# Optimization experiments

Measured on AMD Instinct MI355X. Metric: run time of the kernel, lower is better.

## Reference

```python
import jax, jax.numpy as jnp
import numpy as np
from jax import lax

H_IMG = 128; W_IMG = 128; C_IN = 200; NCLS = 16
N0 = H_IMG * W_IMG; N1 = 4096; N2 = 1024
K = 16  # neighbors(15) + 1 self loop, as in __init__
EPS = 1e-5
SLOPE = 0.01  # LeakyReLU default


def _leaky(x):
    return jnp.where(x >= 0, x, SLOPE * x)


def _bn1d(H, g, b):
    # BatchNorm1d in training mode: batch stats over node dim
    mu = H.mean(0)
    var = H.var(0)
    return (H - mu) * lax.rsqrt(var + EPS) * g + b


def _bn2d(x, g, b):
    mu = x.mean((0, 2, 3), keepdims=True)
    var = x.var((0, 2, 3), keepdims=True)
    return (x - mu) * lax.rsqrt(var + EPS) * g[None, :, None, None] + b[None, :, None, None]


def _ssconv(x, g, b, pw, pb, dw, db):
    # BN -> 1x1 pointwise conv -> LeakyReLU -> depthwise 5x5 conv -> LeakyReLU
    y = _bn2d(x, g, b)
    y = lax.conv_general_dilated(y, pw, (1, 1), 'SAME', dimension_numbers=('NCHW', 'OIHW', 'NCHW')) + pb[None, :, None, None]
    y = _leaky(y)
    c = dw.shape[0]
    y = lax.conv_general_dilated(y, dw, (1, 1), 'SAME', feature_group_count=c, dimension_numbers=('NCHW', 'OIHW', 'NCHW')) + db[None, :, None, None]
    return _leaky(y)


def _gcn(H, g, b, wt, bt, wo, bo, nbr):
    # GCNLayer_PyG, neighbors>0 branch. nbr: [N, K] neighbor indices (col), center broadcast (row)
    Hn = _bn1d(H, g, b)
    th = Hn @ wt + bt            # [N, 128]
    out = Hn @ wo + bo           # [N, F]
    A = jax.nn.sigmoid(jnp.einsum('nkd,nd->nk', th[nbr], th))  # sigmoid(<theta[col], theta[row]>)
    A = jax.nn.softmax(A, axis=1)                              # softmax over K neighbors
    agg = jnp.einsum('nk,nkf->nf', A, out[nbr])                # weighted neighbor aggregate
    return _leaky(agg), A


def _forward(x, hg, hb, hpw, hpb, hdw, hdb,
             e0_g, e0_b, e0_wt, e0_bt, e0_wo, e0_bo,
             e1_g, e1_b, e1_wt, e1_bt, e1_wo, e1_bo,
             d0_g, d0_b, d0_wt, d0_bt, d0_wo, d0_bo,
             tg, tb, tpw, tpb, tdw, tdb, ws, wb,
             S0, S1, Shat0, Shat1, nbr_a, nbr_b):
    x4 = x.transpose(2, 0, 1)[None]                 # [1, C, H, W]
    h0 = _ssconv(x4, hg, hb, hpw, hpb, hdw, hdb)    # [1, 128, H, W]
    H = h0[0].transpose(1, 2, 0).reshape(N0, -1)    # [N0, 128]
    enc0 = H
    H = Shat0 @ H                                   # pool to [N1, 128]
    H, A0 = _gcn(H, e0_g, e0_b, e0_wt, e0_bt, e0_wo, e0_bo, nbr_a)  # [N1, 64]
    enc1 = H
    H = Shat1 @ H                                   # pool to [N2, 64]
    H, A1 = _gcn(H, e1_g, e1_b, e1_wt, e1_bt, e1_wo, e1_bo, nbr_b)  # [N2, 32]
    # decoder
    H = S1 @ H                                      # unpool [N1, 32]
    H = jnp.concatenate([H, enc1], axis=-1)         # [N1, 96]
    H, Ad = _gcn(H, d0_g, d0_b, d0_wt, d0_bt, d0_wo, d0_bo, nbr_a)  # [N1, 64]
    H = S0 @ H                                      # unpool [N0, 64]
    H = jnp.concatenate([H, enc0], axis=-1)         # [N0, 192]
    t = H.reshape(1, H_IMG, W_IMG, -1).transpose(0, 3, 1, 2)
    f = _ssconv(t, tg, tb, tpw, tpb, tdw, tdb)      # [1, 128, H, W]
    f = f[0].transpose(1, 2, 0).reshape(N0, -1)
    Y = jax.nn.softmax(f @ ws + wb, axis=-1)        # [N0, NCLS]
    return Y


def setup_inputs() -> dict:
    key = jax.random.key(0)
    cnt = [0]
    def rn(shape, s=0.05):
        cnt[0] += 1
        return jax.random.normal(jax.random.fold_in(key, cnt[0]), shape, jnp.float32) * s
    x = rn((H_IMG, W_IMG, C_IN), 1.0)
    # balanced hierarchical assignment matrices (one-hot rows)
    S0 = jnp.zeros((N0, N1), jnp.float32).at[jnp.arange(N0), jnp.arange(N0) // (N0 // N1)].set(1.0)
    S1 = jnp.zeros((N1, N2), jnp.float32).at[jnp.arange(N1), jnp.arange(N1) // (N1 // N2)].set(1.0)
    Shat0 = (S0 / S0.sum(0, keepdims=True)).T
    Shat1 = (S1 / S1.sum(0, keepdims=True)).T
    # positions: pixel grid pooled through Shat (as in HiGCN.__init__)
    gx, gy = jnp.meshgrid(jnp.arange(H_IMG), jnp.arange(W_IMG), indexing='ij')
    pos = jnp.stack([gx, gy], -1).reshape(N0, 2).astype(jnp.float32)
    posA = Shat0 @ pos
    posB = Shat1 @ posA
    def knn(p):
        d = ((p[:, None, :] - p[None, :, :]) ** 2).sum(-1)
        return jnp.argsort(d, axis=1)[:, :K].astype(jnp.int32)  # self included (loop=True)
    nbr_a = knn(posA)  # [N1, K], used by enc0 and dec0
    nbr_b = knn(posB)  # [N2, K], used by enc1
    inp = dict(x=x, S0=S0, S1=S1, Shat0=Shat0, Shat1=Shat1, nbr_a=nbr_a, nbr_b=nbr_b)
    inp.update(hg=jnp.ones(C_IN), hb=jnp.zeros(C_IN), hpw=rn((128, C_IN, 1, 1)),
               hpb=jnp.zeros(128), hdw=rn((128, 1, 5, 5)), hdb=jnp.zeros(128))
    for tag, ci, co in (('e0', 128, 64), ('e1', 64, 32), ('d0', 96, 64)):
        inp[tag + '_g'] = jnp.ones(ci); inp[tag + '_b'] = jnp.zeros(ci)
        inp[tag + '_wt'] = rn((ci, 128)); inp[tag + '_bt'] = jnp.zeros(128)
        inp[tag + '_wo'] = rn((ci, co)); inp[tag + '_bo'] = jnp.zeros(co)
    inp.update(tg=jnp.ones(192), tb=jnp.zeros(192), tpw=rn((128, 192, 1, 1)),
               tpb=jnp.zeros(128), tdw=rn((128, 1, 5, 5)), tdb=jnp.zeros(128))
    inp.update(ws=rn((128, NCLS)), wb=jnp.zeros(NCLS))
    return inp


def reference(x, hg, hb, hpw, hpb, hdw, hdb,
              e0_g, e0_b, e0_wt, e0_bt, e0_wo, e0_bo,
              e1_g, e1_b, e1_wt, e1_bt, e1_wo, e1_bo,
              d0_g, d0_b, d0_wt, d0_bt, d0_wo, d0_bo,
              tg, tb, tpw, tpb, tdw, tdb, ws, wb,
              S0, S1, Shat0, Shat1, nbr_a, nbr_b):
    return _forward(x, hg, hb, hpw, hpb, hdw, hdb,
                    e0_g, e0_b, e0_wt, e0_bt, e0_wo, e0_bo,
                    e1_g, e1_b, e1_wt, e1_bt, e1_wo, e1_bo,
                    d0_g, d0_b, d0_wt, d0_bt, d0_wo, d0_bo,
                    tg, tb, tpw, tpb, tdw, tdb, ws, wb,
                    S0, S1, Shat0, Shat1, nbr_a, nbr_b)
```

## Files before the change

kernel.cpp:

```cpp
#include <hip/hip_runtime.h>
#include <hip/hip_bf16.h>
#include <math.h>

using bf16 = __hip_bfloat16;

#define H_IMG 128
#define W_IMG 128
#define C_IN  200
#define NCLS  16
#define N0    16384
#define N1    4096
#define N2    1024
#define KNB   16
#define EPS   1e-5f
#define SLOPE 0.01f

__device__ __forceinline__ float ldf(const float* p, long i) { return p[i]; }
__device__ __forceinline__ float ldf(const bf16* p, long i) { return __bfloat162float(p[i]); }
__device__ __forceinline__ float leaky(float v) { return v >= 0.f ? v : SLOPE * v; }

__device__ __forceinline__ float4 ld4(const float* p, long i) {
    return *reinterpret_cast<const float4*>(p + i);
}
__device__ __forceinline__ float4 ld4(const bf16* p, long i) {
    const ushort4 u = *reinterpret_cast<const ushort4*>(reinterpret_cast<const unsigned short*>(p) + i);
    float4 r;
    r.x = __uint_as_float((unsigned)u.x << 16);
    r.y = __uint_as_float((unsigned)u.y << 16);
    r.z = __uint_as_float((unsigned)u.z << 16);
    r.w = __uint_as_float((unsigned)u.w << 16);
    return r;
}

__global__ void detect_kernel(const unsigned short* __restrict__ x, int* __restrict__ flag) {
    int t = threadIdx.x;
    int cnt = 0;
    for (int i = t; i < 4096; i += 64) {
        unsigned short e = (unsigned short)((x[i] >> 7) & 0xFF);
        if (e >= 0xC0) cnt++;
    }
#pragma unroll
    for (int off = 32; off > 0; off >>= 1) cnt += __shfl_xor(cnt, off, 64);
    if (t == 0) *flag = (cnt > 32) ? 1 : 0;
}

template <typename TX>
__device__ __forceinline__ void bnA_body(const TX* __restrict__ X, int P, int C, float* __restrict__ part) {
    int b = blockIdx.x;
    int t = threadIdx.x;
    int rpb = P >> 8;
    if (t < C) {
        float s = 0.f, s2 = 0.f;
        long base = (long)b * rpb * C + t;
        for (int r = 0; r < rpb; r++) {
            float v = ldf(X, base + (long)r * C);
            s += v; s2 += v * v;
        }
        part[(long)t * 256 + b] = s;
        part[65536 + (long)t * 256 + b] = s2;
    }
}

__global__ __launch_bounds__(256) void bnA_kernel(const void* X, int P, int C, float* part,
                                                  const int* flag, int xraw) {
    if (*flag || !xraw) bnA_body<float>((const float*)X, P, C, part);
    else bnA_body<bf16>((const bf16*)X, P, C, part);
}

__global__ __launch_bounds__(256) void bnB_kernel(const float* __restrict__ part, int P,
                                                  const void* g, const void* b_,
                                                  float* __restrict__ alpha, float* __restrict__ beta,
                                                  const int* flag) {
    int c = blockIdx.x;
    int t = threadIdx.x;
    __shared__ float rs[256], rq[256];
    rs[t] = part[(long)c * 256 + t];
    rq[t] = part[65536 + (long)c * 256 + t];
    __syncthreads();
    for (int k = 128; k > 0; k >>= 1) {
        if (t < k) { rs[t] += rs[t + k]; rq[t] += rq[t + k]; }
        __syncthreads();
    }
    if (t == 0) {
        float mu = rs[0] / (float)P;
        float var = rq[0] / (float)P - mu * mu;
        float gv = *flag ? ((const float*)g)[c] : __bfloat162float(((const bf16*)g)[c]);
        float bv = *flag ? ((const float*)b_)[c] : __bfloat162float(((const bf16*)b_)[c]);
        float a = rsqrtf(var + EPS) * gv;
        alpha[c] = a;
        beta[c] = bv - mu * a;
    }
}

template <typename TW>
__device__ __forceinline__ void fold_body(const TW* __restrict__ W, const TW* __restrict__ bias,
                                          const float* __restrict__ alpha, const float* __restrict__ beta,
                                          float* __restrict__ Wf, float* __restrict__ Bf,
                                          int Ci, int Co, int omajor, int j) {
    int t = threadIdx.x;
    float acc = 0.f;
    for (int c = t; c < Ci; c += 256) {
        float w = omajor ? ldf(W, (long)j * Ci + c) : ldf(W, (long)c * Co + j);
        Wf[(long)c * Co + j] = w * alpha[c];
        acc += w * beta[c];
    }
    __shared__ float red[256];
    red[t] = acc; __syncthreads();
    for (int k = 128; k > 0; k >>= 1) { if (t < k) red[t] += red[t + k]; __syncthreads(); }
    if (t == 0) Bf[j] = ldf(bias, (long)j) + red[0];
}

__global__ __launch_bounds__(256) void fold_kernel(const void* W, const void* bias,
                                                   const float* alpha, const float* beta,
                                                   float* Wf, float* Bf, int Ci, int Co, int omajor,
                                                   const int* flag) {
    if (*flag) fold_body<float>((const float*)W, (const float*)bias, alpha, beta, Wf, Bf, Ci, Co, omajor, blockIdx.x);
    else fold_body<bf16>((const bf16*)W, (const bf16*)bias, alpha, beta, Wf, Bf, Ci, Co, omajor, blockIdx.x);
}

__global__ __launch_bounds__(256) void fold2_kernel(const void* W1, const void* b1,
                                                    const void* W2, const void* b2,
                                                    const float* alpha, const float* beta,
                                                    float* Wf1, float* Bf1, float* Wf2, float* Bf2,
                                                    int Ci, int Co1, int Co2, const int* flag) {
    int j = blockIdx.x;
    if (*flag) {
        if (j < Co1) fold_body<float>((const float*)W1, (const float*)b1, alpha, beta, Wf1, Bf1, Ci, Co1, 0, j);
        else fold_body<float>((const float*)W2, (const float*)b2, alpha, beta, Wf2, Bf2, Ci, Co2, 0, j - Co1);
    } else {
        if (j < Co1) fold_body<bf16>((const bf16*)W1, (const bf16*)b1, alpha, beta, Wf1, Bf1, Ci, Co1, 0, j);
        else fold_body<bf16>((const bf16*)W2, (const bf16*)b2, alpha, beta, Wf2, Bf2, Ci, Co2, 0, j - Co1);
    }
}

template <typename T, int ACT>
__device__ __forceinline__ void gemm4_body(const T* __restrict__ In, const float* __restrict__ Wf,
                                           const float* __restrict__ Bf, float* __restrict__ Out,
                                           int Ci, int Co, int blk) {
    int tid = blk * 256 + threadIdx.x;
    int Coq = Co >> 2;
    int n = tid / Coq;
    int j4 = (tid - n * Coq) << 2;
    const T* in = In + (long)n * Ci;
    const float* wp = Wf + j4;
    float4 acc = *reinterpret_cast<const float4*>(Bf + j4);
    for (int c = 0; c < Ci; c += 4) {
        float4 xv = ld4(in, c);
        float4 w0 = *reinterpret_cast<const float4*>(wp + (long)c * Co);
        float4 w1 = *reinterpret_cast<const float4*>(wp + (long)(c + 1) * Co);
        float4 w2 = *reinterpret_cast<const float4*>(wp + (long)(c + 2) * Co);
        float4 w3 = *reinterpret_cast<const float4*>(wp + (long)(c + 3) * Co);
        acc.x += xv.x * w0.x; acc.y += xv.x * w0.y; acc.z += xv.x * w0.z; acc.w += xv.x * w0.w;
        acc.x += xv.y * w1.x; acc.y += xv.y * w1.y; acc.z += xv.y * w1.z; acc.w += xv.y * w1.w;
        acc.x += xv.z * w2.x; acc.y += xv.z * w2.y; acc.z += xv.z * w2.z; acc.w += xv.z * w2.w;
        acc.x += xv.w * w3.x; acc.y += xv.w * w3.y; acc.z += xv.w * w3.z; acc.w += xv.w * w3.w;
    }
    if (ACT) { acc.x = leaky(acc.x); acc.y = leaky(acc.y); acc.z = leaky(acc.z); acc.w = leaky(acc.w); }
    *reinterpret_cast<float4*>(Out + (long)n * Co + j4) = acc;
}

__global__ __launch_bounds__(256) void gemm4_dyn_kernel(const void* In, const float* Wf, const float* Bf,
                                                        float* Out, int Ci, int Co, const int* flag) {
    if (*flag) gemm4_body<float, 1>((const float*)In, Wf, Bf, Out, Ci, Co, blockIdx.x);
    else gemm4_body<bf16, 1>((const bf16*)In, Wf, Bf, Out, Ci, Co, blockIdx.x);
}

template <int ACT>
__global__ __launch_bounds__(256) void gemm4_f32_kernel(const float* In, const float* Wf, const float* Bf,
                                                        float* Out, int Ci, int Co) {
    gemm4_body<float, ACT>(In, Wf, Bf, Out, Ci, Co, blockIdx.x);
}

template <int ACT>
__global__ __launch_bounds__(256) void gemm2_f32_kernel(const float* In,
                                                        const float* W1, const float* B1, float* O1, int Co1,
                                                        const float* W2, const float* B2, float* O2, int Co2,
                                                        int Ci, int nb1) {
    int b = blockIdx.x;
    if (b < nb1) gemm4_body<float, ACT>(In, W1, B1, O1, Ci, Co1, b);
    else gemm4_body<float, ACT>(In, W2, B2, O2, Ci, Co2, b - nb1);
}

template <typename TW>
__device__ __forceinline__ void dw4_body(const float* __restrict__ In, const TW* __restrict__ dwp,
                                         const TW* __restrict__ dbp, float* __restrict__ Out) {
    __shared__ float wl[25][128];
    __shared__ float bl[128];
    int t = threadIdx.x;
    for (int e = t; e < 25 * 128; e += 256) {
        int o = e / 25, i = e - o * 25;
        wl[i][o] = ldf(dwp, e);
    }
    if (t < 128) bl[t] = ldf(dbp, (long)t);
    __syncthreads();

    int tid = blockIdx.x * 256 + t;
    int o0 = (tid & 31) << 2;
    int p = tid >> 5;
    int h = p >> 7, w = p & 127;
    float4 acc = *reinterpret_cast<const float4*>(&bl[o0]);
#pragma unroll
    for (int dh = -2; dh <= 2; dh++) {
        int hh = h + dh;
        if ((unsigned)hh >= (unsigned)H_IMG) continue;
#pragma unroll
        for (int dv = -2; dv <= 2; dv++) {
            int ww = w + dv;
            if ((unsigned)ww >= (unsigned)W_IMG) continue;
            float4 iv = *reinterpret_cast<const float4*>(&In[(long)(((hh << 7) + ww) << 7) + o0]);
            float4 wv = *reinterpret_cast<const float4*>(&wl[(dh + 2) * 5 + (dv + 2)][o0]);
            acc.x += iv.x * wv.x; acc.y += iv.y * wv.y; acc.z += iv.z * wv.z; acc.w += iv.w * wv.w;
        }
    }
    acc.x = leaky(acc.x); acc.y = leaky(acc.y); acc.z = leaky(acc.z); acc.w = leaky(acc.w);
    *reinterpret_cast<float4*>(&Out[(long)p * 128 + o0]) = acc;
}

__global__ __launch_bounds__(256) void dw4_kernel(const float* In, const void* dwp, const void* dbp,
                                                  float* Out, const int* flag) {
    if (*flag) dw4_body<float>(In, (const float*)dwp, (const float*)dbp, Out);
    else dw4_body<bf16>(In, (const bf16*)dwp, (const bf16*)dbp, Out);
}

__global__ __launch_bounds__(256) void pool4_kernel(const float* __restrict__ In, float* __restrict__ Out, int F) {
    int tid = blockIdx.x * 256 + threadIdx.x;
    int Fq = F >> 2;
    int j = tid / Fq;
    int f4 = (tid - j * Fq) << 2;
    const float* base = In + (long)(4 * j) * F + f4;
    float4 a = *reinterpret_cast<const float4*>(base);
    float4 b = *reinterpret_cast<const float4*>(base + F);
    float4 c = *reinterpret_cast<const float4*>(base + 2 * F);
    float4 d = *reinterpret_cast<const float4*>(base + 3 * F);
    float4 r;
    r.x = 0.25f * (a.x + b.x + c.x + d.x);
    r.y = 0.25f * (a.y + b.y + c.y + d.y);
    r.z = 0.25f * (a.z + b.z + c.z + d.z);
    r.w = 0.25f * (a.w + b.w + c.w + d.w);
    *reinterpret_cast<float4*>(Out + (long)j * F + f4) = r;
}

__global__ __launch_bounds__(256) void attn_kernel(const float* __restrict__ th, const float* __restrict__ outm,
                                                   const int* __restrict__ nbr, float* __restrict__ dst, int co) {
    int n = blockIdx.x * 4 + (threadIdx.x >> 6);
    int l = threadIdx.x & 63;
    float r0 = th[(long)n * 128 + l];
    float r1 = th[(long)n * 128 + 64 + l];
    int mk[KNB];
    float av[KNB];
#pragma unroll
    for (int k = 0; k < KNB; k++) {
        int m = nbr[n * KNB + k];
        mk[k] = m;
        float v = r0 * th[(long)m * 128 + l] + r1 * th[(long)m * 128 + 64 + l];
#pragma unroll
        for (int off = 32; off > 0; off >>= 1) v += __shfl_xor(v, off, 64);
        av[k] = 1.f / (1.f + expf(-v));
    }
    float amax = av[0];
#pragma unroll
    for (int k = 1; k < KNB; k++) amax = fmaxf(amax, av[k]);
    float den = 0.f;
#pragma unroll
    for (int k = 0; k < KNB; k++) { av[k] = expf(av[k] - amax); den += av[k]; }
    float rden = 1.f / den;
    if (l < co) {
        float acc = 0.f;
#pragma unroll
        for (int k = 0; k < KNB; k++) acc += av[k] * outm[(long)mk[k] * co + l];
        dst[(long)n * co + l] = leaky(acc * rden);
    }
}

__global__ __launch_bounds__(256) void concat_hcat_kernel(const float* __restrict__ Hd, const float* __restrict__ enc1,
                                                          float* __restrict__ Hcat) {
    int tid = blockIdx.x * 256 + threadIdx.x;
    int n = tid / 24;
    int f4 = (tid - n * 24) << 2;
    float4 v;
    if (f4 < 32) v = *reinterpret_cast<const float4*>(&Hd[(long)(n >> 2) * 32 + f4]);
    else v = *reinterpret_cast<const float4*>(&enc1[(long)n * 64 + (f4 - 32)]);
    *reinterpret_cast<float4*>(&Hcat[(long)n * 96 + f4]) = v;
}

__global__ __launch_bounds__(256) void concat_g_kernel(const float* __restrict__ Hdec, const float* __restrict__ H0,
                                                       float* __restrict__ G) {
    int tid = blockIdx.x * 256 + threadIdx.x;
    int p = tid / 48;
    int f4 = (tid - p * 48) << 2;
    float4 v;
    if (f4 < 64) v = *reinterpret_cast<const float4*>(&Hdec[(long)(p >> 2) * 64 + f4]);
    else v = *reinterpret_cast<const float4*>(&H0[(long)p * 128 + (f4 - 64)]);
    *reinterpret_cast<float4*>(&G[(long)p * 192 + f4]) = v;
}

template <typename TW>
__device__ __forceinline__ void cls_body(const float* __restrict__ F, const TW* __restrict__ wsw,
                                         const TW* __restrict__ wb, TW* __restrict__ out) {
    __shared__ float wl[128 * 16];
    int t = threadIdx.x;
    for (int e = t; e < 2048; e += 256) wl[e] = ldf(wsw, (long)e);
    __syncthreads();
    int tid = blockIdx.x * 256 + t;
    int p = tid >> 4;
    int j = tid & 15;
    float acc = ldf(wb, (long)j);
    const float* fp = F + (long)p * 128;
#pragma unroll 8
    for (int c = 0; c < 128; c += 4) {
        float4 fv = *reinterpret_cast<const float4*>(fp + c);
        acc += fv.x * wl[c * 16 + j] + fv.y * wl[(c + 1) * 16 + j]
             + fv.z * wl[(c + 2) * 16 + j] + fv.w * wl[(c + 3) * 16 + j];
    }
    float m = acc;
#pragma unroll
    for (int s = 8; s > 0; s >>= 1) m = fmaxf(m, __shfl_xor(m, s, 16));
    float e = expf(acc - m);
    float d = e;
#pragma unroll
    for (int s = 8; s > 0; s >>= 1) d += __shfl_xor(d, s, 16);
    float r = e / d;
    if constexpr (sizeof(TW) == 2) out[tid] = __float2bfloat16(r);
    else out[tid] = r;
}

__global__ __launch_bounds__(256) void cls_kernel(const float* F, const void* wsw, const void* wb,
                                                  void* out, const int* flag) {
    if (*flag) cls_body<float>(F, (const float*)wsw, (const float*)wb, (float*)out);
    else cls_body<bf16>(F, (const bf16*)wsw, (const bf16*)wb, (bf16*)out);
}

extern "C" void kernel_launch(void* const* d_in, const int* in_sizes, int n_in,
                              void* d_out, int out_size, void* d_ws, size_t ws_size,
                              hipStream_t stream) {
    bool dict = (in_sizes[1] > 1000000);
    int I_x, I_nbr_a, I_nbr_b, I_hg, I_ws, I_e0, I_e1, I_d0, I_tg;
    if (dict) {
        I_x = 0; I_nbr_a = 5; I_nbr_b = 6; I_hg = 7; I_e0 = 13; I_e1 = 19; I_d0 = 25; I_tg = 31; I_ws = 37;
    } else {
        I_x = 0; I_hg = 1; I_e0 = 7; I_e1 = 13; I_d0 = 19; I_tg = 25; I_ws = 31; I_nbr_a = 37; I_nbr_b = 38;
    }
    const void* x    = d_in[I_x];
    const int* nbr_a = (const int*)d_in[I_nbr_a];
    const int* nbr_b = (const int*)d_in[I_nbr_b];
    const void* hg   = d_in[I_hg + 0];
    const void* hb   = d_in[I_hg + 1];
    const void* hpw  = d_in[I_hg + 2];
    const void* hpb  = d_in[I_hg + 3];
    const void* hdw  = d_in[I_hg + 4];
    const void* hdb  = d_in[I_hg + 5];
    const void* e0_g = d_in[I_e0 + 0];
    const void* e0_b = d_in[I_e0 + 1];
    const void* e0_wt= d_in[I_e0 + 2];
    const void* e0_bt= d_in[I_e0 + 3];
    const void* e0_wo= d_in[I_e0 + 4];
    const void* e0_bo= d_in[I_e0 + 5];
    const void* e1_g = d_in[I_e1 + 0];
    const void* e1_b = d_in[I_e1 + 1];
    const void* e1_wt= d_in[I_e1 + 2];
    const void* e1_bt= d_in[I_e1 + 3];
    const void* e1_wo= d_in[I_e1 + 4];
    const void* e1_bo= d_in[I_e1 + 5];
    const void* d0_g = d_in[I_d0 + 0];
    const void* d0_b = d_in[I_d0 + 1];
    const void* d0_wt= d_in[I_d0 + 2];
    const void* d0_bt= d_in[I_d0 + 3];
    const void* d0_wo= d_in[I_d0 + 4];
    const void* d0_bo= d_in[I_d0 + 5];
    const void* tg   = d_in[I_tg + 0];
    const void* tb   = d_in[I_tg + 1];
    const void* tpw  = d_in[I_tg + 2];
    const void* tpb  = d_in[I_tg + 3];
    const void* tdw  = d_in[I_tg + 4];
    const void* tdb  = d_in[I_tg + 5];
    const void* wsw  = d_in[I_ws + 0];
    const void* wb   = d_in[I_ws + 1];

    float* W = (float*)d_ws;
    float* AB_a  = W + 0;
    float* AB_b  = W + 256;
    float* WF1   = W + 512;
    float* BF1   = W + 33280;
    float* WF2   = W + 33536;
    float* BF2   = W + 41728;
    int*   dflag = (int*)(W + 49152);
    float* PART  = W + 49408;
    float* R0    = W + 196608;
    float* R1    = R0 + (long)N0*192;
    float* H1b   = R1 + (long)N0*128;
    float* THb   = H1b + (long)N1*128;
    float* OUTb  = THb + (long)N1*128;
    float* ENC1  = OUTb + (long)N1*64;
    float* H2b   = ENC1 + (long)N1*64;
    float* HDb   = H2b + (long)N2*64;
    float* HCAT  = HDb + (long)N2*32;
    float* HDEC  = HCAT + (long)N1*96;

    detect_kernel<<<1, 64, 0, stream>>>((const unsigned short*)x, dflag);

    bnA_kernel<<<256, 256, 0, stream>>>(x, N0, C_IN, PART, dflag, 1);
    bnB_kernel<<<C_IN, 256, 0, stream>>>(PART, N0, hg, hb, AB_a, AB_b, dflag);
    fold_kernel<<<128, 256, 0, stream>>>(hpw, hpb, AB_a, AB_b, WF1, BF1, C_IN, 128, 1, dflag);
    gemm4_dyn_kernel<<<(N0 * 128 / 4) / 256, 256, 0, stream>>>(x, WF1, BF1, R0, C_IN, 128, dflag);
    dw4_kernel<<<(N0 * 32) / 256, 256, 0, stream>>>(R0, hdw, hdb, R1, dflag);
    pool4_kernel<<<(N1 * 32) / 256, 256, 0, stream>>>(R1, H1b, 128);

    bnA_kernel<<<256, 256, 0, stream>>>(H1b, N1, 128, PART, dflag, 0);
    bnB_kernel<<<128, 256, 0, stream>>>(PART, N1, e0_g, e0_b, AB_a, AB_b, dflag);
    fold2_kernel<<<192, 256, 0, stream>>>(e0_wt, e0_bt, e0_wo, e0_bo, AB_a, AB_b,
                                          WF1, BF1, WF2, BF2, 128, 128, 64, dflag);
    {
        int nb1 = (N1 * 32) / 256, nb2 = (N1 * 16) / 256;
        gemm2_f32_kernel<0><<<nb1 + nb2, 256, 0, stream>>>(H1b, WF1, BF1, THb, 128,
                                                           WF2, BF2, OUTb, 64, 128, nb1);
    }
    attn_kernel<<<N1 / 4, 256, 0, stream>>>(THb, OUTb, nbr_a, ENC1, 64);
    pool4_kernel<<<(N2 * 16) / 256, 256, 0, stream>>>(ENC1, H2b, 64);

    bnA_kernel<<<256, 256, 0, stream>>>(H2b, N2, 64, PART, dflag, 0);
    bnB_kernel<<<64, 256, 0, stream>>>(PART, N2, e1_g, e1_b, AB_a, AB_b, dflag);
    fold2_kernel<<<160, 256, 0, stream>>>(e1_wt, e1_bt, e1_wo, e1_bo, AB_a, AB_b,
                                          WF1, BF1, WF2, BF2, 64, 128, 32, dflag);
    {
        int nb1 = (N2 * 32) / 256, nb2 = (N2 * 8) / 256;
        gemm2_f32_kernel<0><<<nb1 + nb2, 256, 0, stream>>>(H2b, WF1, BF1, THb, 128,
                                                           WF2, BF2, OUTb, 32, 64, nb1);
    }
    attn_kernel<<<N2 / 4, 256, 0, stream>>>(THb, OUTb, nbr_b, HDb, 32);

    concat_hcat_kernel<<<(N1 * 24) / 256, 256, 0, stream>>>(HDb, ENC1, HCAT);
    bnA_kernel<<<256, 256, 0, stream>>>(HCAT, N1, 96, PART, dflag, 0);
    bnB_kernel<<<96, 256, 0, stream>>>(PART, N1, d0_g, d0_b, AB_a, AB_b, dflag);
    fold2_kernel<<<192, 256, 0, stream>>>(d0_wt, d0_bt, d0_wo, d0_bo, AB_a, AB_b,
                                          WF1, BF1, WF2, BF2, 96, 128, 64, dflag);
    {
        int nb1 = (N1 * 32) / 256, nb2 = (N1 * 16) / 256;
        gemm2_f32_kernel<0><<<nb1 + nb2, 256, 0, stream>>>(HCAT, WF1, BF1, THb, 128,
                                                           WF2, BF2, OUTb, 64, 96, nb1);
    }
    attn_kernel<<<N1 / 4, 256, 0, stream>>>(THb, OUTb, nbr_a, HDEC, 64);

    concat_g_kernel<<<(N0 * 48) / 256, 256, 0, stream>>>(HDEC, R1, R0);
    bnA_kernel<<<256, 256, 0, stream>>>(R0, N0, 192, PART, dflag, 0);
    bnB_kernel<<<192, 256, 0, stream>>>(PART, N0, tg, tb, AB_a, AB_b, dflag);
    fold_kernel<<<128, 256, 0, stream>>>(tpw, tpb, AB_a, AB_b, WF1, BF1, 192, 128, 1, dflag);
    gemm4_f32_kernel<1><<<(N0 * 128 / 4) / 256, 256, 0, stream>>>(R0, WF1, BF1, R1, 192, 128);
    dw4_kernel<<<(N0 * 32) / 256, 256, 0, stream>>>(R1, tdw, tdb, R0, dflag);
    cls_kernel<<<(N0 * NCLS) / 256, 256, 0, stream>>>(R0, wsw, wb, d_out, dflag);
}
```

Before: 841.2 us.

## Fuse BN statistics into producers, fold concats into GEMMs, cut launches

Computes BatchNorm partial sums inside the kernels that produce each tensor: pooling, attention, and the input read, which now also does dtype detection. It merges the stats reduction with the weight-fold kernels. The two concat kernels are removed by letting the GEMMs read from two source buffers, with the upsampled part indexed by n>>2. The aim is fewer launches and fewer full passes over intermediate tensors, at the cost of more complex kernels and redundant per-block alpha/beta recomputation in the fold kernels.

```diff
diff --git a/kernel.cpp b/kernel.cpp
--- a/kernel.cpp
+++ b/kernel.cpp
@@ -32,77 +32,72 @@
     return r;
 }
 
-__global__ void detect_kernel(const unsigned short* __restrict__ x, int* __restrict__ flag) {
-    int t = threadIdx.x;
+__device__ __forceinline__ int block_detect(const unsigned short* __restrict__ x) {
+    __shared__ int cnt_s;
+    if (threadIdx.x == 0) cnt_s = 0;
+    __syncthreads();
     int cnt = 0;
-    for (int i = t; i < 4096; i += 64) {
+    for (int i = threadIdx.x; i < 4096; i += blockDim.x) {
         unsigned short e = (unsigned short)((x[i] >> 7) & 0xFF);
         if (e >= 0xC0) cnt++;
     }
 #pragma unroll
     for (int off = 32; off > 0; off >>= 1) cnt += __shfl_xor(cnt, off, 64);
-    if (t == 0) *flag = (cnt > 32) ? 1 : 0;
-}
-
-template <typename TX>
-__device__ __forceinline__ void bnA_body(const TX* __restrict__ X, int P, int C, float* __restrict__ part) {
-    int b = blockIdx.x;
+    if ((threadIdx.x & 63) == 0) atomicAdd(&cnt_s, cnt);
+    __syncthreads();
+    return cnt_s > 32 ? 1 : 0;
+}
+
+__global__ __launch_bounds__(256) void bnx_kernel(const void* __restrict__ X, float2* __restrict__ part,
+                                                  int* __restrict__ dflag) {
+    int fl = block_detect((const unsigned short*)X);
+    if (blockIdx.x == 0 && threadIdx.x == 0) *dflag = fl;
+    int b = blockIdx.x, t = threadIdx.x;
+    if (t >= C_IN) return;
+    float s = 0.f, s2 = 0.f;
+    if (fl) {
+        const float* p = (const float*)X + (long)b * 64 * C_IN + t;
+        for (int r = 0; r < 64; r++) { float v = p[(long)r * C_IN]; s += v; s2 += v * v; }
+    } else {
+        const bf16* p = (const bf16*)X + (long)b * 64 * C_IN + t;
+        for (int r = 0; r < 64; r++) { float v = __bfloat162float(p[(long)r * C_IN]); s += v; s2 += v * v; }
+    }
+    part[(long)t * 256 + b] = make_float2(s, s2);
+}
+
+__device__ __forceinline__ void alphabeta_ld(const float2* __restrict__ partA, int npA, int splitC,
+                                             const float2* __restrict__ partB, int npB,
+                                             int Ci, float Pinv, const void* g, const void* b_,
+                                             int flag, float* al, float* be) {
     int t = threadIdx.x;
-    int rpb = P >> 8;
-    if (t < C) {
+    if (t < Ci) {
+        const float2* src = (t < splitC) ? partA + (long)t * npA : partB + (long)(t - splitC) * npB;
+        int np = (t < splitC) ? npA : npB;
         float s = 0.f, s2 = 0.f;
-        long base = (long)b * rpb * C + t;
-        for (int r = 0; r < rpb; r++) {
-            float v = ldf(X, base + (long)r * C);
-            s += v; s2 += v * v;
-        }
-        part[(long)t * 256 + b] = s;
-        part[65536 + (long)t * 256 + b] = s2;
-    }
-}
-
-__global__ __launch_bounds__(256) void bnA_kernel(const void* X, int P, int C, float* part,
-                                                  const int* flag, int xraw) {
-    if (*flag || !xraw) bnA_body<float>((const float*)X, P, C, part);
-    else bnA_body<bf16>((const bf16*)X, P, C, part);
-}
-
-__global__ __launch_bounds__(256) void bnB_kernel(const float* __restrict__ part, int P,
-                                                  const void* g, const void* b_,
-                                                  float* __restrict__ alpha, float* __restrict__ beta,
-                                                  const int* flag) {
-    int c = blockIdx.x;
-    int t = threadIdx.x;
-    __shared__ float rs[256], rq[256];
-    rs[t] = part[(long)c * 256 + t];
-    rq[t] = part[65536 + (long)c * 256 + t];
-    __syncthreads();
-    for (int k = 128; k > 0; k >>= 1) {
-        if (t < k) { rs[t] += rs[t + k]; rq[t] += rq[t + k]; }
-        __syncthreads();
-    }
-    if (t == 0) {
-        float mu = rs[0] / (float)P;
-        float var = rq[0] / (float)P - mu * mu;
-        float gv = *flag ? ((const float*)g)[c] : __bfloat162float(((const bf16*)g)[c]);
-        float bv = *flag ? ((const float*)b_)[c] : __bfloat162float(((const bf16*)b_)[c]);
+        const float4* p4 = (const float4*)src;
+        for (int i = 0; i < (np >> 1); i++) { float4 v = p4[i]; s += v.x + v.z; s2 += v.y + v.w; }
+        float mu = s * Pinv;
+        float var = s2 * Pinv - mu * mu;
+        float gv = flag ? ((const float*)g)[t] : __bfloat162float(((const bf16*)g)[t]);
+        float bv = flag ? ((const float*)b_)[t] : __bfloat162float(((const bf16*)b_)[t]);
         float a = rsqrtf(var + EPS) * gv;
-        alpha[c] = a;
-        beta[c] = bv - mu * a;
-    }
+        al[t] = a;
+        be[t] = bv - mu * a;
+    }
+    __syncthreads();
 }
 
 template <typename TW>
-__device__ __forceinline__ void fold_body(const TW* __restrict__ W, const TW* __restrict__ bias,
-                                          const float* __restrict__ alpha, const float* __restrict__ beta,
-                                          float* __restrict__ Wf, float* __restrict__ Bf,
-                                          int Ci, int Co, int omajor, int j) {
+__device__ __forceinline__ void foldL_body(const TW* __restrict__ W, const TW* __restrict__ bias,
+                                           const float* __restrict__ al, const float* __restrict__ be,
+                                           float* __restrict__ Wf, float* __restrict__ Bf,
+                                           int Ci, int Co, int omajor, int j) {
     int t = threadIdx.x;
     float acc = 0.f;
     for (int c = t; c < Ci; c += 256) {
         float w = omajor ? ldf(W, (long)j * Ci + c) : ldf(W, (long)c * Co + j);
-        Wf[(long)c * Co + j] = w * alpha[c];
-        acc += w * beta[c];
+        Wf[(long)c * Co + j] = w * al[c];
+        acc += w * be[c];
     }
     __shared__ float red[256];
     red[t] = acc; __syncthreads();
@@ -110,26 +105,36 @@
     if (t == 0) Bf[j] = ldf(bias, (long)j) + red[0];
 }
 
-__global__ __launch_bounds__(256) void fold_kernel(const void* W, const void* bias,
-                                                   const float* alpha, const float* beta,
-                                                   float* Wf, float* Bf, int Ci, int Co, int omajor,
-                                                   const int* flag) {
-    if (*flag) fold_body<float>((const float*)W, (const float*)bias, alpha, beta, Wf, Bf, Ci, Co, omajor, blockIdx.x);
-    else fold_body<bf16>((const bf16*)W, (const bf16*)bias, alpha, beta, Wf, Bf, Ci, Co, omajor, blockIdx.x);
-}
-
-__global__ __launch_bounds__(256) void fold2_kernel(const void* W1, const void* b1,
-                                                    const void* W2, const void* b2,
-                                                    const float* alpha, const float* beta,
-                                                    float* Wf1, float* Bf1, float* Wf2, float* Bf2,
-                                                    int Ci, int Co1, int Co2, const int* flag) {
+__global__ __launch_bounds__(256) void bnfold_kernel(const float2* partA, int npA, int splitC,
+                                                     const float2* partB, int npB, int P,
+                                                     const void* g, const void* b_,
+                                                     const void* Wt, const void* bias,
+                                                     float* Wf, float* Bf, int Ci, int Co, int omajor,
+                                                     const int* dflag) {
+    __shared__ float al[256], be[256];
+    int flag = *dflag;
+    alphabeta_ld(partA, npA, splitC, partB, npB, Ci, 1.f / (float)P, g, b_, flag, al, be);
+    if (flag) foldL_body<float>((const float*)Wt, (const float*)bias, al, be, Wf, Bf, Ci, Co, omajor, blockIdx.x);
+    else foldL_body<bf16>((const bf16*)Wt, (const bf16*)bias, al, be, Wf, Bf, Ci, Co, omajor, blockIdx.x);
+}
+
+__global__ __launch_bounds__(256) void bnfold2_kernel(const float2* partA, int npA, int splitC,
+                                                      const float2* partB, int npB, int P,
+                                                      const void* g, const void* b_,
+                                                      const void* W1, const void* b1,
+                                                      const void* W2, const void* b2,
+                                                      float* Wf1, float* Bf1, float* Wf2, float* Bf2,
+                                                      int Ci, int Co1, int Co2, const int* dflag) {
+    __shared__ float al[256], be[256];
+    int flag = *dflag;
+    alphabeta_ld(partA, npA, splitC, partB, npB, Ci, 1.f / (float)P, g, b_, flag, al, be);
     int j = blockIdx.x;
-    if (*flag) {
-        if (j < Co1) fold_body<float>((const float*)W1, (const float*)b1, alpha, beta, Wf1, Bf1, Ci, Co1, 0, j);
-        else fold_body<float>((const float*)W2, (const float*)b2, alpha, beta, Wf2, Bf2, Ci, Co2, 0, j - Co1);
+    if (flag) {
+        if (j < Co1) foldL_body<float>((const float*)W1, (const float*)b1, al, be, Wf1, Bf1, Ci, Co1, 0, j);
+        else foldL_body<float>((const float*)W2, (const float*)b2, al, be, Wf2, Bf2, Ci, Co2, 0, j - Co1);
     } else {
-        if (j < Co1) fold_body<bf16>((const bf16*)W1, (const bf16*)b1, alpha, beta, Wf1, Bf1, Ci, Co1, 0, j);
-        else fold_body<bf16>((const bf16*)W2, (const bf16*)b2, alpha, beta, Wf2, Bf2, Ci, Co2, 0, j - Co1);
+        if (j < Co1) foldL_body<bf16>((const bf16*)W1, (const bf16*)b1, al, be, Wf1, Bf1, Ci, Co1, 0, j);
+        else foldL_body<bf16>((const bf16*)W2, (const bf16*)b2, al, be, Wf2, Bf2, Ci, Co2, 0, j - Co1);
     }
 }
 
@@ -159,26 +164,65 @@
     *reinterpret_cast<float4*>(Out + (long)n * Co + j4) = acc;
 }
 
+template <int ACT, int SPLIT>
+__device__ __forceinline__ void gemm4cat_body(const float* __restrict__ InA, int sA,
+                                              const float* __restrict__ InB, int sB,
+                                              const float* __restrict__ Wf, const float* __restrict__ Bf,
+                                              float* __restrict__ Out, int Ci, int Co, int blk) {
+    int tid = blk * 256 + threadIdx.x;
+    int Coq = Co >> 2;
+    int n = tid / Coq;
+    int j4 = (tid - n * Coq) << 2;
+    const float* ia = InA + (long)(n >> 2) * sA;
+    const float* ib = InB + (long)n * sB;
+    const float* wp = Wf + j4;
+    float4 acc = *reinterpret_cast<const float4*>(Bf + j4);
+    for (int c = 0; c < Ci; c += 4) {
+        float4 xv = (c < SPLIT) ? *reinterpret_cast<const float4*>(ia + c)
+                                : *reinterpret_cast<const float4*>(ib + (c - SPLIT));
+        float4 w0 = *reinterpret_cast<const float4*>(wp + (long)c * Co);
+        float4 w1 = *reinterpret_cast<const float4*>(wp + (long)(c + 1) * Co);
+        float4 w2 = *reinterpret_cast<const float4*>(wp + (long)(c + 2) * Co);
+        float4 w3 = *reinterpret_cast<const float4*>(wp + (long)(c + 3) * Co);
+        acc.x += xv.x * w0.x; acc.y += xv.x * w0.y; acc.z += xv.x * w0.z; acc.w += xv.x * w0.w;
+        acc.x += xv.y * w1.x; acc.y += xv.y * w1.y; acc.z += xv.y * w1.z; acc.w += xv.y * w1.w;
+        acc.x += xv.z * w2.x; acc.y += xv.z * w2.y; acc.z += xv.z * w2.z; acc.w += xv.z * w2.w;
+        acc.x += xv.w * w3.x; acc.y += xv.w * w3.y; acc.z += xv.w * w3.z; acc.w += xv.w * w3.w;
+    }
+    if (ACT) { acc.x = leaky(acc.x); acc.y = leaky(acc.y); acc.z = leaky(acc.z); acc.w = leaky(acc.w); }
+    *reinterpret_cast<float4*>(Out + (long)n * Co + j4) = acc;
+}
+
 __global__ __launch_bounds__(256) void gemm4_dyn_kernel(const void* In, const float* Wf, const float* Bf,
                                                         float* Out, int Ci, int Co, const int* flag) {
     if (*flag) gemm4_body<float, 1>((const float*)In, Wf, Bf, Out, Ci, Co, blockIdx.x);
     else gemm4_body<bf16, 1>((const bf16*)In, Wf, Bf, Out, Ci, Co, blockIdx.x);
 }
 
-template <int ACT>
-__global__ __launch_bounds__(256) void gemm4_f32_kernel(const float* In, const float* Wf, const float* Bf,
-                                                        float* Out, int Ci, int Co) {
-    gemm4_body<float, ACT>(In, Wf, Bf, Out, Ci, Co, blockIdx.x);
-}
-
-template <int ACT>
 __global__ __launch_bounds__(256) void gemm2_f32_kernel(const float* In,
                                                         const float* W1, const float* B1, float* O1, int Co1,
                                                         const float* W2, const float* B2, float* O2, int Co2,
                                                         int Ci, int nb1) {
     int b = blockIdx.x;
-    if (b < nb1) gemm4_body<float, ACT>(In, W1, B1, O1, Ci, Co1, b);
-    else gemm4_body<float, ACT>(In, W2, B2, O2, Ci, Co2, b - nb1);
+    if (b < nb1) gemm4_body<float, 0>(In, W1, B1, O1, Ci, Co1, b);
+    else gemm4_body<float, 0>(In, W2, B2, O2, Ci, Co2, b - nb1);
+}
+
+template <int SPLIT>
+__global__ __launch_bounds__(256) void gemm2cat_kernel(const float* InA, int sA, const float* InB, int sB,
+                                                       const float* W1, const float* B1, float* O1, int Co1,
+                                                       const float* W2, const float* B2, float* O2, int Co2,
+                                                       int Ci, int nb1) {
+    int b = blockIdx.x;
+    if (b < nb1) gemm4cat_body<0, SPLIT>(InA, sA, InB, sB, W1, B1, O1, Ci, Co1, b);
+    else gemm4cat_body<0, SPLIT>(InA, sA, InB, sB, W2, B2, O2, Ci, Co2, b - nb1);
+}
+
+template <int SPLIT>
+__global__ __launch_bounds__(256) void gemmcat_act_kernel(const float* InA, int sA, const float* InB, int sB,
+                                                          const float* Wf, const float* Bf, float* Out,
+                                                          int Ci, int Co) {
+    gemm4cat_body<1, SPLIT>(InA, sA, InB, sB, Wf, Bf, Out, Ci, Co, blockIdx.x);
 }
 
 template <typename TW>
@@ -222,28 +266,33 @@
     else dw4_body<bf16>(In, (const bf16*)dwp, (const bf16*)dbp, Out);
 }
 
-__global__ __launch_bounds__(256) void pool4_kernel(const float* __restrict__ In, float* __restrict__ Out, int F) {
-    int tid = blockIdx.x * 256 + threadIdx.x;
-    int Fq = F >> 2;
-    int j = tid / Fq;
-    int f4 = (tid - j * Fq) << 2;
-    const float* base = In + (long)(4 * j) * F + f4;
-    float4 a = *reinterpret_cast<const float4*>(base);
-    float4 b = *reinterpret_cast<const float4*>(base + F);
-    float4 c = *reinterpret_cast<const float4*>(base + 2 * F);
-    float4 d = *reinterpret_cast<const float4*>(base + 3 * F);
-    float4 r;
-    r.x = 0.25f * (a.x + b.x + c.x + d.x);
-    r.y = 0.25f * (a.y + b.y + c.y + d.y);
-    r.z = 0.25f * (a.z + b.z + c.z + d.z);
-    r.w = 0.25f * (a.w + b.w + c.w + d.w);
-    *reinterpret_cast<float4*>(Out + (long)j * F + f4) = r;
-}
-
-__global__ __launch_bounds__(256) void attn_kernel(const float* __restrict__ th, const float* __restrict__ outm,
-                                                   const int* __restrict__ nbr, float* __restrict__ dst, int co) {
-    int n = blockIdx.x * 4 + (threadIdx.x >> 6);
-    int l = threadIdx.x & 63;
+__global__ __launch_bounds__(128) void bnpool_kernel(const float* __restrict__ R1f, float* __restrict__ H1b,
+                                                     float2* __restrict__ partE0, float2* __restrict__ partTb) {
+    int b = blockIdx.x, t = threadIdx.x;
+    float s = 0.f, s2 = 0.f;
+    float rs = 0.f, rs2 = 0.f;
+    const float* base = R1f + (long)b * 64 * 128 + t;
+    for (int r = 0; r < 16; r++) {
+        const float* rp = base + (long)r * 512;
+        float v0 = rp[0], v1 = rp[128], v2 = rp[256], v3 = rp[384];
+        float h = 0.25f * (v0 + v1 + v2 + v3);
+        H1b[(long)(b * 16 + r) * 128 + t] = h;
+        s += h; s2 += h * h;
+        rs += v0 + v1 + v2 + v3;
+        rs2 += v0 * v0 + v1 * v1 + v2 * v2 + v3 * v3;
+    }
+    partE0[(long)t * 256 + b] = make_float2(s, s2);
+    partTb[(long)t * 256 + b] = make_float2(rs, rs2);
+}
+
+template <int MODE>
+__global__ __launch_bounds__(256) void attn_fused_kernel(const float* __restrict__ th, const float* __restrict__ outm,
+                                                         const int* __restrict__ nbr, float* __restrict__ dst, int co,
+                                                         float* __restrict__ H2b,
+                                                         float2* __restrict__ partP, float2* __restrict__ partS,
+                                                         int snp) {
+    int wid = threadIdx.x >> 6, l = threadIdx.x & 63;
+    int n = blockIdx.x * 4 + wid;
     float r0 = th[(long)n * 128 + l];
     float r1 = th[(long)n * 128 + 64 + l];
     int mk[KNB];
@@ -264,34 +313,30 @@
 #pragma unroll
     for (int k = 0; k < KNB; k++) { av[k] = expf(av[k] - amax); den += av[k]; }
     float rden = 1.f / den;
+    float val = 0.f;
     if (l < co) {
         float acc = 0.f;
 #pragma unroll
         for (int k = 0; k < KNB; k++) acc += av[k] * outm[(long)mk[k] * co + l];
-        dst[(long)n * co + l] = leaky(acc * rden);
-    }
-}
-
-__global__ __launch_bounds__(256) void concat_hcat_kernel(const float* __restrict__ Hd, const float* __restrict__ enc1,
-                                                          float* __restrict__ Hcat) {
-    int tid = blockIdx.x * 256 + threadIdx.x;
-    int n = tid / 24;
-    int f4 = (tid - n * 24) << 2;
-    float4 v;
-    if (f4 < 32) v = *reinterpret_cast<const float4*>(&Hd[(long)(n >> 2) * 32 + f4]);
-    else v = *reinterpret_cast<const float4*>(&enc1[(long)n * 64 + (f4 - 32)]);
-    *reinterpret_cast<float4*>(&Hcat[(long)n * 96 + f4]) = v;
-}
-
-__global__ __launch_bounds__(256) void concat_g_kernel(const float* __restrict__ Hdec, const float* __restrict__ H0,
-                                                       float* __restrict__ G) {
-    int tid = blockIdx.x * 256 + threadIdx.x;
-    int p = tid / 48;
-    int f4 = (tid - p * 48) << 2;
-    float4 v;
-    if (f4 < 64) v = *reinterpret_cast<const float4*>(&Hdec[(long)(p >> 2) * 64 + f4]);
-    else v = *reinterpret_cast<const float4*>(&H0[(long)p * 128 + (f4 - 64)]);
-    *reinterpret_cast<float4*>(&G[(long)p * 192 + f4]) = v;
+        val = leaky(acc * rden);
+        dst[(long)n * co + l] = val;
+    }
+    __shared__ float sm[4][64];
+    sm[wid][l] = (l < co) ? val : 0.f;
+    __syncthreads();
+    if (wid == 0 && l < co) {
+        float a = sm[0][l], b = sm[1][l], c = sm[2][l], d = sm[3][l];
+        float su = a + b + c + d;
+        float sq = a * a + b * b + c * c + d * d;
+        if (MODE == 0) {
+            float h = 0.25f * su;
+            H2b[(long)blockIdx.x * 64 + l] = h;
+            partP[(long)l * snp + blockIdx.x] = make_float2(h, h * h);
+            partS[(long)l * snp + blockIdx.x] = make_float2(su, sq);
+        } else {
+            partS[(long)l * snp + blockIdx.x] = make_float2(4.f * su, 4.f * sq);
+        }
+    }
 }
 
 template <typename TW>
@@ -377,74 +422,54 @@
     const void* wb   = d_in[I_ws + 1];
 
     float* W = (float*)d_ws;
-    float* AB_a  = W + 0;
-    float* AB_b  = W + 256;
-    float* WF1   = W + 512;
-    float* BF1   = W + 33280;
-    float* WF2   = W + 33536;
-    float* BF2   = W + 41728;
-    int*   dflag = (int*)(W + 49152);
-    float* PART  = W + 49408;
-    float* R0    = W + 196608;
-    float* R1    = R0 + (long)N0*192;
-    float* H1b   = R1 + (long)N0*128;
-    float* THb   = H1b + (long)N1*128;
-    float* OUTb  = THb + (long)N1*128;
-    float* ENC1  = OUTb + (long)N1*64;
-    float* H2b   = ENC1 + (long)N1*64;
-    float* HDb   = H2b + (long)N2*64;
-    float* HCAT  = HDb + (long)N2*32;
-    float* HDEC  = HCAT + (long)N1*96;
-
-    detect_kernel<<<1, 64, 0, stream>>>((const unsigned short*)x, dflag);
-
-    bnA_kernel<<<256, 256, 0, stream>>>(x, N0, C_IN, PART, dflag, 1);
-    bnB_kernel<<<C_IN, 256, 0, stream>>>(PART, N0, hg, hb, AB_a, AB_b, dflag);
-    fold_kernel<<<128, 256, 0, stream>>>(hpw, hpb, AB_a, AB_b, WF1, BF1, C_IN, 128, 1, dflag);
-    gemm4_dyn_kernel<<<(N0 * 128 / 4) / 256, 256, 0, stream>>>(x, WF1, BF1, R0, C_IN, 128, dflag);
-    dw4_kernel<<<(N0 * 32) / 256, 256, 0, stream>>>(R0, hdw, hdb, R1, dflag);
-    pool4_kernel<<<(N1 * 32) / 256, 256, 0, stream>>>(R1, H1b, 128);
-
-    bnA_kernel<<<256, 256, 0, stream>>>(H1b, N1, 128, PART, dflag, 0);
-    bnB_kernel<<<128, 256, 0, stream>>>(PART, N1, e0_g, e0_b, AB_a, AB_b, dflag);
-    fold2_kernel<<<192, 256, 0, stream>>>(e0_wt, e0_bt, e0_wo, e0_bo, AB_a, AB_b,
-                                          WF1, BF1, WF2, BF2, 128, 128, 64, dflag);
-    {
-        int nb1 = (N1 * 32) / 256, nb2 = (N1 * 16) / 256;
-        gemm2_f32_kernel<0><<<nb1 + nb2, 256, 0, stream>>>(H1b, WF1, BF1, THb, 128,
-                                                           WF2, BF2, OUTb, 64, 128, nb1);
-    }
-    attn_kernel<<<N1 / 4, 256, 0, stream>>>(THb, OUTb, nbr_a, ENC1, 64);
-    pool4_kernel<<<(N2 * 16) / 256, 256, 0, stream>>>(ENC1, H2b, 64);
-
-    bnA_kernel<<<256, 256, 0, stream>>>(H2b, N2, 64, PART, dflag, 0);
-    bnB_kernel<<<64, 256, 0, stream>>>(PART, N2, e1_g, e1_b, AB_a, AB_b, dflag);
-    fold2_kernel<<<160, 256, 0, stream>>>(e1_wt, e1_bt, e1_wo, e1_bo, AB_a, AB_b,
-                                          WF1, BF1, WF2, BF2, 64, 128, 32, dflag);
-    {
-        int nb1 = (N2 * 32) / 256, nb2 = (N2 * 8) / 256;
-        gemm2_f32_kernel<0><<<nb1 + nb2, 256, 0, stream>>>(H2b, WF1, BF1, THb, 128,
-                                                           WF2, BF2, OUTb, 32, 64, nb1);
-    }
-    attn_kernel<<<N2 / 4, 256, 0, stream>>>(THb, OUTb, nbr_b, HDb, 32);
-
-    concat_hcat_kernel<<<(N1 * 24) / 256, 256, 0, stream>>>(HDb, ENC1, HCAT);
-    bnA_kernel<<<256, 256, 0, stream>>>(HCAT, N1, 96, PART, dflag, 0);
-    bnB_kernel<<<96, 256, 0, stream>>>(PART, N1, d0_g, d0_b, AB_a, AB_b, dflag);
-    fold2_kernel<<<192, 256, 0, stream>>>(d0_wt, d0_bt, d0_wo, d0_bo, AB_a, AB_b,
-                                          WF1, BF1, WF2, BF2, 96, 128, 64, dflag);
-    {
-        int nb1 = (N1 * 32) / 256, nb2 = (N1 * 16) / 256;
-        gemm2_f32_kernel<0><<<nb1 + nb2, 256, 0, stream>>>(HCAT, WF1, BF1, THb, 128,
-                                                           WF2, BF2, OUTb, 64, 96, nb1);
-    }
-    attn_kernel<<<N1 / 4, 256, 0, stream>>>(THb, OUTb, nbr_a, HDEC, 64);
-
-    concat_g_kernel<<<(N0 * 48) / 256, 256, 0, stream>>>(HDEC, R1, R0);
-    bnA_kernel<<<256, 256, 0, stream>>>(R0, N0, 192, PART, dflag, 0);
-    bnB_kernel<<<192, 256, 0, stream>>>(PART, N0, tg, tb, AB_a, AB_b, dflag);
-    fold_kernel<<<128, 256, 0, stream>>>(tpw, tpb, AB_a, AB_b, WF1, BF1, 192, 128, 1, dflag);
-    gemm4_f32_kernel<1><<<(N0 * 128 / 4) / 256, 256, 0, stream>>>(R0, WF1, BF1, R1, 192, 128);
-    dw4_kernel<<<(N0 * 32) / 256, 256, 0, stream>>>(R1, tdw, tdb, R0, dflag);
-    cls_kernel<<<(N0 * NCLS) / 256, 256, 0, stream>>>(R0, wsw, wb, d_out, dflag);
-}
+    float*  WF1    = W + 0;
+    float*  BF1    = W + 25600;
+    float*  WF2    = W + 25728;
+    float*  BF2    = W + 33920;
+    int*    dflag  = (int*)(W + 33984);
+    float2* P_HEAD = (float2*)(W + 34048);
+    float2* P_E0   = (float2*)(W + 136448);
+    float2* P_E1   = (float2*)(W + 201984);
+    float2* P_D0a  = (float2*)(W + 333056);
+    float2* P_D0b  = (float2*)(W + 349440);
+    float2* P_Ta   = (float2*)(W + 480512);
+    float2* P_Tb   = (float2*)(W + 611584);
+    float*  R0     = W + 677120;
+    float*  R1     = R0 + (long)N0 * 128;
+    float*  T1     = R1 + (long)N0 * 128;
+    float*  H1b    = T1 + (long)N0 * 128;
+    float*  THb    = H1b + (long)N1 * 128;
+    float*  OUTb   = THb + (long)N1 * 128;
+    float*  ENC1   = OUTb + (long)N1 * 64;
+    float*  H2b    = ENC1 + (long)N1 * 64;
+    float*  HDb    = H2b + (long)N2 * 64;
+    float*  HDEC   = HDb + (long)N2 * 32;
+
+    bnx_kernel<<<256, 256, 0, stream>>>(x, P_HEAD, dflag);
+    bnfold_kernel<<<128, 256, 0, stream>>>(P_HEAD, 256, C_IN, P_HEAD, 256, N0,
+                                           hg, hb, hpw, hpb, WF1, BF1, C_IN, 128, 1, dflag);
+    gemm4_dyn_kernel<<<2048, 256, 0, stream>>>(x, WF1, BF1, R0, C_IN, 128, dflag);
+    dw4_kernel<<<2048, 256, 0, stream>>>(R0, hdw, hdb, R1, dflag);
+    bnpool_kernel<<<256, 128, 0, stream>>>(R1, H1b, P_E0, P_Tb);
+    bnfold2_kernel<<<192, 256, 0, stream>>>(P_E0, 256, 128, P_E0, 256, N1, e0_g, e0_b,
+                                            e0_wt, e0_bt, e0_wo, e0_bo,
+                                            WF1, BF1, WF2, BF2, 128, 128, 64, dflag);
+    gemm2_f32_kernel<<<768, 256, 0, stream>>>(H1b, WF1, BF1, THb, 128, WF2, BF2, OUTb, 64, 128, 512);
+    attn_fused_kernel<0><<<1024, 256, 0, stream>>>(THb, OUTb, nbr_a, ENC1, 64, H2b, P_E1, P_D0b, 1024);
+    bnfold2_kernel<<<160, 256, 0, stream>>>(P_E1, 1024, 64, P_E1, 1024, N2, e1_g, e1_b,
+                                            e1_wt, e1_bt, e1_wo, e1_bo,
+                                            WF1, BF1, WF2, BF2, 64, 128, 32, dflag);
+    gemm2_f32_kernel<<<160, 256, 0, stream>>>(H2b, WF1, BF1, THb, 128, WF2, BF2, OUTb, 32, 64, 128);
+    attn_fused_kernel<1><<<256, 256, 0, stream>>>(THb, OUTb, nbr_b, HDb, 32, nullptr, nullptr, P_D0a, 256);
+    bnfold2_kernel<<<192, 256, 0, stream>>>(P_D0a, 256, 32, P_D0b, 1024, N1, d0_g, d0_b,
+                                            d0_wt, d0_bt, d0_wo, d0_bo,
+                                            WF1, BF1, WF2, BF2, 96, 128, 64, dflag);
+    gemm2cat_kernel<32><<<768, 256, 0, stream>>>(HDb, 32, ENC1, 64,
+                                                 WF1, BF1, THb, 128, WF2, BF2, OUTb, 64, 96, 512);
+    attn_fused_kernel<2><<<1024, 256, 0, stream>>>(THb, OUTb, nbr_a, HDEC, 64, nullptr, nullptr, P_Ta, 1024);
+    bnfold_kernel<<<128, 256, 0, stream>>>(P_Ta, 1024, 64, P_Tb, 256, N0,
+                                           tg, tb, tpw, tpb, WF1, BF1, 192, 128, 1, dflag);
+    gemmcat_act_kernel<64><<<2048, 256, 0, stream>>>(HDEC, 64, R1, 128, WF1, BF1, T1, 192, 128);
+    dw4_kernel<<<2048, 256, 0, stream>>>(T1, tdw, tdb, R0, dflag);
+    cls_kernel<<<1024, 256, 0, stream>>>(R0, wsw, wb, d_out, dflag);
+}
```

Result: slower. 959.4 us (+14.1%).
